# Kernel tuning notes

Measured on AMD Instinct MI355X. Metric: run time of the kernel, lower is better.

## Reference

```python
import jax, jax.numpy as jnp
import numpy as np

N, E, DIM, L, NPERM, B = 20000, 640000, 128, 4, 20000, 256
R = NPERM * L * L  # rows of perm matrices
EPS = 1e-5


def _mlp(x, w1, b1, g, beta, w2, b2):
    # Linear -> BatchNorm (training-mode batch stats) -> ReLU -> Linear
    h = x @ w1 + b1
    mu = h.mean(0)
    var = h.var(0)  # biased, matches torch BN normalization
    h = (h - mu) * jax.lax.rsqrt(var + EPS) * g + beta
    return jax.nn.relu(h) @ w2 + b2


def setup_inputs() -> dict:
    key = jax.random.key(0)
    ks = jax.random.split(key, 40)
    s = 0.05
    inp = {}
    inp["node_feat"] = jax.random.normal(ks[0], (N, DIM), jnp.float32)
    inp["edge_feat"] = jax.random.normal(ks[1], (E, DIM), jnp.float32)
    inp["src"] = jax.random.randint(ks[2], (E,), 0, N)
    inp["dst"] = jax.random.randint(ks[3], (E,), 0, N)
    inp["rev_flag"] = jax.random.randint(ks[4], (E,), 0, 2).astype(bool)
    # sparse node_to_perm / edge_to_perm: one nnz per row (row i implicit)
    inp["n2p_cols"] = jax.random.randint(ks[5], (R,), 0, N)
    inp["n2p_vals"] = jax.random.uniform(ks[6], (R,), jnp.float32)
    inp["e2p_cols"] = jax.random.randint(ks[7], (R,), 0, E)
    inp["e2p_vals"] = jax.random.uniform(ks[8], (R,), jnp.float32)
    # sparse pooling matrix: perm j -> graph pool_rows[j] with weight pool_vals[j]
    inp["pool_rows"] = jax.random.randint(ks[9], (NPERM,), 0, B)
    inp["pool_vals"] = jax.random.uniform(ks[10], (NPERM,), jnp.float32)
    for i, n in enumerate(["in_w", "out_w", "src_w", "dst_w", "nloop_w", "eloop_w"]):
        inp[n] = jax.random.normal(ks[11 + i], (DIM, DIM), jnp.float32) * s
    inp["lrp_w"] = jax.random.normal(ks[17], (DIM, DIM, L * L), jnp.float32) * s
    inp["nbias"] = jnp.zeros((DIM,), jnp.float32)
    inp["ebias"] = jnp.zeros((DIM,), jnp.float32)
    inp["lrp_bias"] = jnp.zeros((DIM,), jnp.float32)
    for p, k0 in (("n", 20), ("e", 26)):
        inp[p + "mlp_w1"] = jax.random.normal(ks[k0], (DIM, DIM), jnp.float32) * s
        inp[p + "mlp_b1"] = jnp.zeros((DIM,), jnp.float32)
        inp[p + "mlp_g"] = jnp.ones((DIM,), jnp.float32)
        inp[p + "mlp_beta"] = jnp.zeros((DIM,), jnp.float32)
        inp[p + "mlp_w2"] = jax.random.normal(ks[k0 + 1], (DIM, DIM), jnp.float32) * s
        inp[p + "mlp_b2"] = jnp.zeros((DIM,), jnp.float32)
    return inp


def reference(node_feat, edge_feat, src, dst, rev_flag, n2p_cols, n2p_vals,
              e2p_cols, e2p_vals, pool_rows, pool_vals,
              in_w, out_w, src_w, dst_w, nloop_w, eloop_w, lrp_w,
              nbias, ebias, lrp_bias,
              nmlp_w1, nmlp_b1, nmlp_g, nmlp_beta, nmlp_w2, nmlp_b2,
              emlp_w1, emlp_b1, emlp_g, emlp_beta, emlp_w2, emlp_b2):
    hs = node_feat[src]   # [E, d]
    hd = node_feat[dst]   # [E, d]
    r = rev_flag[:, None]
    # per-edge messages with reverse-edge masking
    edge_msg = jnp.where(r, hs @ dst_w - hd @ src_w, hd @ dst_w - hs @ src_w)
    node_msg = jnp.where(r, edge_feat @ out_w, -(edge_feat @ in_w))
    node_agg = jax.ops.segment_sum(node_msg, dst, num_segments=N)
    # node update
    nout = _mlp(node_feat @ nloop_w + node_agg + nbias,
                nmlp_w1, nmlp_b1, nmlp_g, nmlp_beta, nmlp_w2, nmlp_b2)
    # edge update: degree-scaled term uses out-degree of dst node
    out_deg = jax.ops.segment_sum(jnp.ones((E,), jnp.float32), src, num_segments=N)
    dlog = jnp.log2(1.0 + out_deg[dst])[:, None]
    add = 2.0 * (1.0 + dlog) * (edge_feat @ (src_w - dst_w))
    eout = _mlp(edge_feat @ eloop_w + add + edge_msg + ebias,
                emlp_w1, emlp_b1, emlp_g, emlp_beta, emlp_w2, emlp_b2)
    # sparse perm gathers + LRP einsum + sparse pooling scatter
    perm = n2p_vals[:, None] * nout[n2p_cols] + e2p_vals[:, None] * eout[e2p_cols]
    perm = perm.reshape(NPERM, L * L, DIM)
    lrp = jnp.einsum('dab,bca->dc', perm, lrp_w) + lrp_bias
    pooled = jax.ops.segment_sum(pool_vals[:, None] * lrp, pool_rows, num_segments=B)
    return pooled, eout
```

## Files before the change

kernel.cpp:

```cpp
#include <hip/hip_runtime.h>
#include <stdint.h>

constexpr int Nn     = 20000;
constexpr int Ee     = 640000;
constexpr int NPERMc = 20000;

using bf16x8 = __attribute__((ext_vector_type(8))) short;
using f32x4  = __attribute__((ext_vector_type(4))) float;
using s16x4  = __attribute__((ext_vector_type(4))) short;
using u16x8  = __attribute__((ext_vector_type(8))) unsigned short;

__device__ __forceinline__ short f2bf(float f) {
  union { float f; unsigned u; } v; v.f = f;
  unsigned r = v.u + 0x7FFFu + ((v.u >> 16) & 1u);
  return (short)(r >> 16);
}
__device__ __forceinline__ float bf2f(unsigned short s) {
  union { unsigned u; float f; } v; v.u = ((unsigned)s) << 16;
  return v.f;
}
__device__ __forceinline__ f32x4 MFMA(bf16x8 a, bf16x8 b, f32x4 c) {
  return __builtin_amdgcn_mfma_f32_16x16x32_bf16(a, b, c, 0, 0, 0);
}

__device__ __forceinline__ int fragIdx(int k, int n) {
  int t = n >> 4, kk = k >> 5;
  int l = ((k & 31) >> 3) * 16 + (n & 15);
  int j = k & 7;
  return ((t * 4 + kk) * 64 + l) * 8 + j;
}

__device__ __forceinline__ void stage16x128(const float* __restrict__ src, int row0, int M,
                                            int lane, short* lds) {
  #pragma unroll
  for (int it = 0; it < 8; ++it) {
    int u = it * 64 + lane;
    int r = u >> 5;
    int q = u & 31;
    int row = row0 + r;
    float4 v = make_float4(0.f, 0.f, 0.f, 0.f);
    if (row < M) v = ((const float4*)(src + (size_t)row * 128))[q];
    int k  = q * 4;
    int kk = k >> 5;
    int l2 = ((k & 31) >> 3) * 16 + r;
    int j  = k & 7;
    s16x4 s4 = { f2bf(v.x), f2bf(v.y), f2bf(v.z), f2bf(v.w) };
    *(s16x4*)(lds + (kk * 64 + l2) * 8 + j) = s4;
  }
}

__global__ __launch_bounds__(256) void kPrep(
    const float* __restrict__ in_w,  const float* __restrict__ out_w,
    const float* __restrict__ src_w, const float* __restrict__ dst_w,
    const float* __restrict__ nloop_w, const float* __restrict__ eloop_w,
    const float* __restrict__ lrp_w,
    const float* __restrict__ nbias, const float* __restrict__ ebias,
    const float* __restrict__ w1e, const float* __restrict__ b1e,
    const float* __restrict__ w1n, const float* __restrict__ b1n,
    const float* __restrict__ w2e, const float* __restrict__ w2n,
    short* __restrict__ WA, short* __restrict__ BQ, short* __restrict__ WN,
    short* __restrict__ W2E, short* __restrict__ W2N, short* __restrict__ WL,
    float* __restrict__ c0e, float* __restrict__ c0n) {
  __shared__ float Rl[16384];
  int tid = threadIdx.x;
  int blk = blockIdx.x;
  if (blk < 448) {
    int p = blk >> 6, sub = blk & 63;
    const float* La; const float* Lb = nullptr; const float* R; short* outp;
    float sOut = 1.f;
    switch (p) {
      case 0: La = eloop_w;             R = w1e; outp = WA;          break;
      case 1: La = src_w; Lb = dst_w;   R = w1e; outp = WA + 16384;  break;
      case 2: La = dst_w;               R = w1e; outp = BQ;          break;
      case 3: La = src_w;               R = w1e; outp = BQ + 16384;  break;
      case 4: La = nloop_w;             R = w1n; outp = WN;          break;
      case 5: La = out_w;               R = w1n; outp = WN + 16384;  break;
      default: La = in_w;               R = w1n; outp = WN + 32768; sOut = -1.f; break;
    }
    for (int i = tid; i < 16384; i += 256) Rl[i] = R[i];
    __syncthreads();
    int e = sub * 256 + tid;
    int k = e >> 7, n = e & 127;
    float acc = 0.f;
    bool hasLb = (Lb != nullptr);
    for (int j = 0; j < 128; ++j) {
      float l = La[k * 128 + j];
      if (hasLb) l -= Lb[k * 128 + j];
      acc += l * Rl[j * 128 + n];
    }
    outp[fragIdx(k, n)] = f2bf(acc * sOut);
  } else if (blk < 512) {
    int e = (blk - 448) * 256 + tid; int k = e >> 7, n = e & 127;
    W2E[fragIdx(k, n)] = f2bf(w2e[k * 128 + n]);
  } else if (blk < 576) {
    int e = (blk - 512) * 256 + tid; int k = e >> 7, n = e & 127;
    W2N[fragIdx(k, n)] = f2bf(w2n[k * 128 + n]);
  } else if (blk < 1600) {
    int q = blk - 576; int a = q >> 6;
    int e = (q & 63) * 256 + tid; int k = e >> 7, n = e & 127;
    WL[a * 16384 + fragIdx(k, n)] = f2bf(lrp_w[(k * 128 + n) * 16 + a]);
  } else {
    if (tid < 128) {
      float acc = 0.f;
      for (int k2 = 0; k2 < 128; ++k2) acc += ebias[k2] * w1e[k2 * 128 + tid];
      c0e[tid] = acc + b1e[tid];
    } else {
      int n = tid - 128; float acc = 0.f;
      for (int k2 = 0; k2 < 128; ++k2) acc += nbias[k2] * w1n[k2 * 128 + n];
      c0n[n] = acc + b1n[n];
    }
  }
}


__global__ __launch_bounds__(256) void kHist(
    const int* __restrict__ srcI, const int* __restrict__ dstI,
    int* __restrict__ cnt, float* __restrict__ deg) {
  int e = blockIdx.x * 256 + threadIdx.x;
  atomicAdd(&cnt[dstI[e]], 1);
  atomicAdd(&deg[srcI[e]], 1.0f);
}

__global__ __launch_bounds__(256) void kScan(const int* __restrict__ cnt,
                                             int* __restrict__ off,
                                             int* __restrict__ cur) {
  __shared__ int lc[Nn];
  __shared__ int ps[256];
  int tid = threadIdx.x;
  for (int i = tid; i < Nn; i += 256) lc[i] = cnt[i];
  __syncthreads();
  constexpr int CH = (Nn + 255) / 256;
  int base = tid * CH;
  int local = 0;
  for (int i = 0; i < CH; ++i) {
    int idx = base + i;
    if (idx < Nn) local += lc[idx];
  }
  ps[tid] = local;
  __syncthreads();
  for (int d = 1; d < 256; d <<= 1) {
    int t = (tid >= d) ? ps[tid - d] : 0;
    __syncthreads();
    if (tid >= d) ps[tid] += t;
    __syncthreads();
  }
  int run = ps[tid] - local;
  for (int i = 0; i < CH; ++i) {
    int idx = base + i;
    if (idx < Nn) { off[idx] = run; cur[idx] = run; run += lc[idx]; }
  }
}

__global__ __launch_bounds__(256) void kScatter(
    const int* __restrict__ dstI, const int* __restrict__ revI,
    int* __restrict__ cur, int* __restrict__ order) {
  int e = blockIdx.x * 256 + threadIdx.x;
  int pos = atomicAdd(&cur[dstI[e]], 1);
  order[pos] = revI[e] ? (e | (int)0x80000000) : e;
}

__global__ __launch_bounds__(256) void kAgg2(
    const float* __restrict__ ef, const int* __restrict__ off,
    const int* __restrict__ cnt, const int* __restrict__ order,
    float* __restrict__ aggR, float* __restrict__ aggN) {
  int w = threadIdx.x >> 6, lane = threadIdx.x & 63;
  int n = blockIdx.x * 4 + w;
  if (n >= Nn) return;
  int s0 = off[n], c = cnt[n];
  float2 aR = make_float2(0.f, 0.f), aN = make_float2(0.f, 0.f);
  int i = 0;
  for (; i + 1 < c; i += 2) {
    int oe0 = order[s0 + i];
    int oe1 = order[s0 + i + 1];
    int e0 = oe0 & 0x7fffffff;
    int e1 = oe1 & 0x7fffffff;
    float2 v0 = ((const float2*)(ef + (size_t)e0 * 128))[lane];
    float2 v1 = ((const float2*)(ef + (size_t)e1 * 128))[lane];
    if (oe0 < 0) { aR.x += v0.x; aR.y += v0.y; } else { aN.x += v0.x; aN.y += v0.y; }
    if (oe1 < 0) { aR.x += v1.x; aR.y += v1.y; } else { aN.x += v1.x; aN.y += v1.y; }
  }
  if (i < c) {
    int oe = order[s0 + i];
    int e = oe & 0x7fffffff;
    float2 v = ((const float2*)(ef + (size_t)e * 128))[lane];
    if (oe < 0) { aR.x += v.x; aR.y += v.y; } else { aN.x += v.x; aN.y += v.y; }
  }
  ((float2*)(aggR + (size_t)n * 128))[lane] = aR;
  ((float2*)(aggN + (size_t)n * 128))[lane] = aN;
}

__global__ __launch_bounds__(256, 2) void kQ(const float* __restrict__ nf,
                                             const short* __restrict__ BQ,
                                             float* __restrict__ Q, int M) {
  __shared__ __align__(16) short alds[4][2048];
  __shared__ __align__(16) short wbuf[8192];
  int tid = threadIdx.x, w = tid >> 6, lane = tid & 63;
  int row0 = blockIdx.x * 64 + w * 16;
  stage16x128(nf, row0, M, lane, alds[w]);
  f32x4 acc[16];
  #pragma unroll
  for (int t = 0; t < 16; ++t) acc[t] = (f32x4){0.f, 0.f, 0.f, 0.f};
  const int4* g4 = (const int4*)BQ;
  for (int kk = 0; kk < 4; ++kk) {
    __syncthreads();
    for (int c = tid; c < 1024; c += 256) {
      int t = c >> 6, l = c & 63;
      ((int4*)wbuf)[c] = g4[(t * 4 + kk) * 64 + l];
    }
    __syncthreads();
    bf16x8 a = *(const bf16x8*)(alds[w] + (kk * 64 + lane) * 8);
    #pragma unroll
    for (int t = 0; t < 16; ++t) {
      bf16x8 b = *(const bf16x8*)(wbuf + (t * 64 + lane) * 8);
      acc[t] = MFMA(a, b, acc[t]);
    }
  }
  int sub = lane >> 4;
  #pragma unroll
  for (int t = 0; t < 16; ++t) {
    int col = t * 16 + (lane & 15);
    #pragma unroll
    for (int i = 0; i < 4; ++i) {
      int row = row0 + sub * 4 + i;
      if (row < M) Q[(size_t)row * 256 + col] = acc[t][i];
    }
  }
}

__global__ __launch_bounds__(256, 2) void kN1(
    const float* __restrict__ nf, const float* __restrict__ aggR,
    const float* __restrict__ aggN, const short* __restrict__ WN,
    const float* __restrict__ c0n, short* __restrict__ hN,
    float* __restrict__ scratchN, int M) {
  __shared__ __align__(16) short alds[4][2048];
  __shared__ __align__(16) short wlds[16384];
  __shared__ float statsLDS[256];
  int tid = threadIdx.x, w = tid >> 6, lane = tid & 63;
  statsLDS[tid] = 0.f;
  int row0 = blockIdx.x * 64 + w * 16;
  f32x4 acc[8];
  #pragma unroll
  for (int t = 0; t < 8; ++t) acc[t] = (f32x4){0.f, 0.f, 0.f, 0.f};
  for (int s = 0; s < 3; ++s) {
    const float* src = (s == 0) ? nf : ((s == 1) ? aggR : aggN);
    __syncthreads();
    const int4* g4 = (const int4*)(WN + s * 16384);
    for (int c = tid; c < 2048; c += 256) ((int4*)wlds)[c] = g4[c];
    __syncthreads();
    stage16x128(src, row0, M, lane, alds[w]);
    for (int kk = 0; kk < 4; ++kk) {
      bf16x8 a = *(const bf16x8*)(alds[w] + (kk * 64 + lane) * 8);
      #pragma unroll
      for (int t = 0; t < 8; ++t) {
        bf16x8 b = *(const bf16x8*)(wlds + ((t * 4 + kk) * 64 + lane) * 8);
        acc[t] = MFMA(a, b, acc[t]);
      }
    }
  }
  int sub = lane >> 4;
  #pragma unroll
  for (int t = 0; t < 8; ++t) {
    int col = t * 16 + (lane & 15);
    float c0 = c0n[col];
    float ss = 0.f, sq = 0.f;
    #pragma unroll
    for (int i = 0; i < 4; ++i) {
      int row = row0 + sub * 4 + i;
      float h = acc[t][i] + c0;
      if (row < M) { hN[(size_t)row * 128 + col] = f2bf(h); ss += h; sq += h * h; }
    }
    ss += __shfl_xor(ss, 16, 64); sq += __shfl_xor(sq, 16, 64);
    ss += __shfl_xor(ss, 32, 64); sq += __shfl_xor(sq, 32, 64);
    if (lane < 16) { atomicAdd(&statsLDS[col], ss); atomicAdd(&statsLDS[128 + col], sq); }
  }
  __syncthreads();
  scratchN[(size_t)tid * gridDim.x + blockIdx.x] = statsLDS[tid];
}

__global__ __launch_bounds__(256, 2) void kD(
    const float* __restrict__ ef, const short* __restrict__ WA,
    const float* __restrict__ Q, const float* __restrict__ c0e,
    const int* __restrict__ srcI, const int* __restrict__ dstI,
    const int* __restrict__ revI, const float* __restrict__ deg,
    short* __restrict__ hE, float* __restrict__ scratchE) {
  __shared__ __align__(16) short alds[4][4096];
  __shared__ __align__(16) short wbuf[4096];
  __shared__ float statsLDS[256];
  int tid = threadIdx.x, w = tid >> 6, lane = tid & 63;
  statsLDS[tid] = 0.f;
  int row0 = blockIdx.x * 128 + w * 32;
  stage16x128(ef, row0,      Ee, lane, alds[w]);
  stage16x128(ef, row0 + 16, Ee, lane, alds[w] + 2048);
  f32x4 acc1[2][8], acc2[2][8];
  #pragma unroll
  for (int g = 0; g < 2; ++g)
    #pragma unroll
    for (int t = 0; t < 8; ++t) { acc1[g][t] = (f32x4){0,0,0,0}; acc2[g][t] = (f32x4){0,0,0,0}; }
  const int4* g4 = (const int4*)WA;
  for (int kk = 0; kk < 4; ++kk) {
    bf16x8 a0 = *(const bf16x8*)(alds[w] + (kk * 64 + lane) * 8);
    bf16x8 a1 = *(const bf16x8*)(alds[w] + 2048 + (kk * 64 + lane) * 8);
    #pragma unroll
    for (int m = 0; m < 2; ++m) {
      __syncthreads();
      for (int c = tid; c < 512; c += 256) {
        int t = c >> 6, l = c & 63;
        ((int4*)wbuf)[c] = g4[m * 2048 + (t * 4 + kk) * 64 + l];
      }
      __syncthreads();
      #pragma unroll
      for (int t = 0; t < 8; ++t) {
        bf16x8 b = *(const bf16x8*)(wbuf + (t * 64 + lane) * 8);
        if (m == 0) { acc1[0][t] = MFMA(a0, b, acc1[0][t]); acc1[1][t] = MFMA(a1, b, acc1[1][t]); }
        else        { acc2[0][t] = MFMA(a0, b, acc2[0][t]); acc2[1][t] = MFMA(a1, b, acc2[1][t]); }
      }
    }
  }
  int sub = lane >> 4;
  #pragma unroll
  for (int g = 0; g < 2; ++g) {
    int rbase = row0 + g * 16;
    int   eIdx[4]; float scl[4]; int qa[4], qb[4];
    #pragma unroll
    for (int i = 0; i < 4; ++i) {
      int e = rbase + sub * 4 + i;
      eIdx[i] = e;
      int s_ = srcI[e], d_ = dstI[e], r_ = revI[e];
      scl[i] = 2.0f * (1.0f + log2f(1.0f + deg[d_]));
      int na = r_ ? s_ : d_;
      int nb = r_ ? d_ : s_;
      qa[i] = na * 256;
      qb[i] = nb * 256 + 128;
    }
    #pragma unroll
    for (int t = 0; t < 8; ++t) {
      int col = t * 16 + (lane & 15);
      float c0 = c0e[col];
      float ss = 0.f, sq = 0.f;
      #pragma unroll
      for (int i = 0; i < 4; ++i) {
        float h = acc1[g][t][i] + scl[i] * acc2[g][t][i]
                + (Q[qa[i] + col] - Q[qb[i] + col]) + c0;
        hE[(size_t)eIdx[i] * 128 + col] = f2bf(h);
        ss += h; sq += h * h;
      }
      ss += __shfl_xor(ss, 16, 64); sq += __shfl_xor(sq, 16, 64);
      ss += __shfl_xor(ss, 32, 64); sq += __shfl_xor(sq, 32, 64);
      if (lane < 16) { atomicAdd(&statsLDS[col], ss); atomicAdd(&statsLDS[128 + col], sq); }
    }
  }
  __syncthreads();
  scratchE[(size_t)tid * gridDim.x + blockIdx.x] = statsLDS[tid];
}

__global__ __launch_bounds__(256) void kFin(const float* __restrict__ scratch, int NB,
                                            float M, const float* __restrict__ g,
                                            const float* __restrict__ beta,
                                            float* __restrict__ st) {
  __shared__ float red[256];
  __shared__ float red2[256];
  int c = blockIdx.x;
  int tid = threadIdx.x;
  float s = 0.f, q = 0.f;
  for (int i = tid; i < NB; i += 256) {
    s += scratch[(size_t)c * NB + i];
    q += scratch[(size_t)(128 + c) * NB + i];
  }
  red[tid] = s; red2[tid] = q;
  __syncthreads();
  for (int off = 128; off > 0; off >>= 1) {
    if (tid < off) { red[tid] += red[tid + off]; red2[tid] += red2[tid + off]; }
    __syncthreads();
  }
  if (tid == 0) {
    float mu  = red[0] / M;
    float var = red2[0] / M - mu * mu;
    float inv = rsqrtf(var + 1e-5f);
    float sc  = g[c] * inv;
    st[c] = sc;
    st[128 + c] = beta[c] - mu * sc;
  }
}

__global__ __launch_bounds__(256, 2) void kF(const short* __restrict__ h,
                                             const float* __restrict__ st,
                                             const short* __restrict__ w2f,
                                             const float* __restrict__ b2,
                                             float* __restrict__ outp, int M) {
  __shared__ __align__(16) short alds[4][2048];
  __shared__ __align__(16) short wlds[16384];
  int tid = threadIdx.x, w = tid >> 6, lane = tid & 63;
  for (int c = tid; c < 2048; c += 256) ((int4*)wlds)[c] = ((const int4*)w2f)[c];
  int row0 = blockIdx.x * 64 + w * 16;
  #pragma unroll
  for (int it = 0; it < 4; ++it) {
    int u = it * 64 + lane;
    int r = u >> 4;
    int c8 = (u & 15) * 8;
    int row = row0 + r;
    u16x8 hv = {0, 0, 0, 0, 0, 0, 0, 0};
    if (row < M) hv = *(const u16x8*)(h + (size_t)row * 128 + c8);
    bf16x8 ov;
    #pragma unroll
    for (int q = 0; q < 8; ++q) {
      float f = bf2f(hv[q]);
      float v = fmaxf(f * st[c8 + q] + st[128 + c8 + q], 0.f);
      ov[q] = f2bf(v);
    }
    int kk = c8 >> 5;
    int l2 = ((c8 & 31) >> 3) * 16 + r;
    *(bf16x8*)(alds[w] + (kk * 64 + l2) * 8) = ov;
  }
  __syncthreads();
  f32x4 acc[8];
  #pragma unroll
  for (int t = 0; t < 8; ++t) acc[t] = (f32x4){0.f, 0.f, 0.f, 0.f};
  for (int kk = 0; kk < 4; ++kk) {
    bf16x8 a = *(const bf16x8*)(alds[w] + (kk * 64 + lane) * 8);
    #pragma unroll
    for (int t = 0; t < 8; ++t) {
      bf16x8 b = *(const bf16x8*)(wlds + ((t * 4 + kk) * 64 + lane) * 8);
      acc[t] = MFMA(a, b, acc[t]);
    }
  }
  int sub = lane >> 4;
  #pragma unroll
  for (int t = 0; t < 8; ++t) {
    int col = t * 16 + (lane & 15);
    float bb = b2[col];
    #pragma unroll
    for (int i = 0; i < 4; ++i) {
      int row = row0 + sub * 4 + i;
      if (row < M) outp[(size_t)row * 128 + col] = acc[t][i] + bb;
    }
  }
}

__global__ __launch_bounds__(256, 2) void kLRP(
    const float* __restrict__ nout, const float* __restrict__ eoutp,
    const int* __restrict__ n2pc, const float* __restrict__ n2pv,
    const int* __restrict__ e2pc, const float* __restrict__ e2pv,
    const int* __restrict__ poolr, const float* __restrict__ poolv,
    const short* __restrict__ WL, const float* __restrict__ lrp_bias,
    float* __restrict__ pooled) {
  __shared__ __align__(16) short alds[4][2048];
  __shared__ __align__(16) short wlds[16384];
  int tid = threadIdx.x, w = tid >> 6, lane = tid & 63;
  int row0 = blockIdx.x * 64 + w * 16;
  f32x4 acc[8];
  #pragma unroll
  for (int t = 0; t < 8; ++t) acc[t] = (f32x4){0.f, 0.f, 0.f, 0.f};
  for (int a = 0; a < 16; ++a) {
    __syncthreads();
    const int4* g4 = (const int4*)(WL + a * 16384);
    for (int c = tid; c < 2048; c += 256) ((int4*)wlds)[c] = g4[c];
    __syncthreads();
    #pragma unroll
    for (int it = 0; it < 8; ++it) {
      int u = it * 64 + lane;
      int r = u >> 5;
      int q = u & 31;
      int d = row0 + r;
      float4 v = make_float4(0.f, 0.f, 0.f, 0.f);
      if (d < NPERMc) {
        int i = d * 16 + a;
        int nc = n2pc[i]; float nv = n2pv[i];
        int ec = e2pc[i]; float ev = e2pv[i];
        float4 nr = ((const float4*)(nout  + (size_t)nc * 128))[q];
        float4 er = ((const float4*)(eoutp + (size_t)ec * 128))[q];
        v.x = nv * nr.x + ev * er.x;
        v.y = nv * nr.y + ev * er.y;
        v.z = nv * nr.z + ev * er.z;
        v.w = nv * nr.w + ev * er.w;
      }
      int k  = q * 4;
      int kk = k >> 5;
      int l2 = ((k & 31) >> 3) * 16 + r;
      int j  = k & 7;
      s16x4 s4 = { f2bf(v.x), f2bf(v.y), f2bf(v.z), f2bf(v.w) };
      *(s16x4*)(alds[w] + (kk * 64 + l2) * 8 + j) = s4;
    }
    for (int kk = 0; kk < 4; ++kk) {
      bf16x8 aa = *(const bf16x8*)(alds[w] + (kk * 64 + lane) * 8);
      #pragma unroll
      for (int t = 0; t < 8; ++t) {
        bf16x8 b = *(const bf16x8*)(wlds + ((t * 4 + kk) * 64 + lane) * 8);
        acc[t] = MFMA(aa, b, acc[t]);
      }
    }
  }
  int sub = lane >> 4;
  #pragma unroll
  for (int t = 0; t < 8; ++t) {
    int col = t * 16 + (lane & 15);
    float lb = lrp_bias[col];
    #pragma unroll
    for (int i = 0; i < 4; ++i) {
      int d = row0 + sub * 4 + i;
      if (d < NPERMc) {
        float val = acc[t][i] + lb;
        atomicAdd(&pooled[poolr[d] * 128 + col], poolv[d] * val);
      }
    }
  }
}

extern "C" void kernel_launch(void* const* d_in, const int* in_sizes, int n_in,
                              void* d_out, int out_size, void* d_ws, size_t ws_size,
                              hipStream_t stream) {
  (void)in_sizes; (void)n_in; (void)out_size; (void)ws_size;
  const float* node_feat = (const float*)d_in[0];
  const float* edge_feat = (const float*)d_in[1];
  const int*   srcI      = (const int*)d_in[2];
  const int*   dstI      = (const int*)d_in[3];
  const int*   revI      = (const int*)d_in[4];
  const int*   n2pc      = (const int*)d_in[5];
  const float* n2pv      = (const float*)d_in[6];
  const int*   e2pc      = (const int*)d_in[7];
  const float* e2pv      = (const float*)d_in[8];
  const int*   poolr     = (const int*)d_in[9];
  const float* poolv     = (const float*)d_in[10];
  const float* in_w      = (const float*)d_in[11];
  const float* out_w     = (const float*)d_in[12];
  const float* src_w     = (const float*)d_in[13];
  const float* dst_w     = (const float*)d_in[14];
  const float* nloop_w   = (const float*)d_in[15];
  const float* eloop_w   = (const float*)d_in[16];
  const float* lrp_w     = (const float*)d_in[17];
  const float* nbias     = (const float*)d_in[18];
  const float* ebias     = (const float*)d_in[19];
  const float* lrp_bias  = (const float*)d_in[20];
  const float* nmlp_w1   = (const float*)d_in[21];
  const float* nmlp_b1   = (const float*)d_in[22];
  const float* nmlp_g    = (const float*)d_in[23];
  const float* nmlp_beta = (const float*)d_in[24];
  const float* nmlp_w2   = (const float*)d_in[25];
  const float* nmlp_b2   = (const float*)d_in[26];
  const float* emlp_w1   = (const float*)d_in[27];
  const float* emlp_b1   = (const float*)d_in[28];
  const float* emlp_g    = (const float*)d_in[29];
  const float* emlp_beta = (const float*)d_in[30];
  const float* emlp_w2   = (const float*)d_in[31];
  const float* emlp_b2   = (const float*)d_in[32];

  float* pooled = (float*)d_out;
  float* eoutp  = (float*)d_out + 32768;

  char* p = (char*)d_ws;
  auto alloc = [&](size_t b) { char* r = p; p += (b + 255) & ~(size_t)255; return r; };
  short* hE   = (short*)alloc((size_t)Ee * 128 * 2);
  float* Qm   = (float*)alloc((size_t)Nn * 256 * 4);
  float* aggR = (float*)alloc((size_t)Nn * 128 * 4);
  float* aggN = (float*)alloc((size_t)Nn * 128 * 4);
  short* hN   = (short*)alloc((size_t)Nn * 128 * 2);
  float* nout = (float*)alloc((size_t)Nn * 128 * 4);
  float* deg  = (float*)alloc((size_t)Nn * 4);
  float* scrE = (float*)alloc((size_t)256 * 5000 * 4);
  float* scrN = (float*)alloc((size_t)256 * 313 * 4);
  float* stE  = (float*)alloc(256 * 4);
  float* stN  = (float*)alloc(256 * 4);
  short* WA   = (short*)alloc(32768 * 2);
  short* BQ   = (short*)alloc(32768 * 2);
  short* WN   = (short*)alloc(49152 * 2);
  short* W2E  = (short*)alloc(16384 * 2);
  short* W2N  = (short*)alloc(16384 * 2);
  short* WL   = (short*)alloc((size_t)16 * 16384 * 2);
  float* c0e  = (float*)alloc(128 * 4);
  float* c0n  = (float*)alloc(128 * 4);
  int*   cnt  = (int*)alloc((size_t)Nn * 4);
  int*   offA = (int*)alloc((size_t)Nn * 4);
  int*   cur  = (int*)alloc((size_t)Nn * 4);
  int*   order= (int*)alloc((size_t)Ee * 4);

  hipMemsetAsync(deg,  0, (size_t)Nn * 4, stream);
  hipMemsetAsync(cnt,  0, (size_t)Nn * 4, stream);
  hipMemsetAsync(pooled, 0, (size_t)32768 * 4, stream);

  kPrep<<<1601, 256, 0, stream>>>(in_w, out_w, src_w, dst_w, nloop_w, eloop_w, lrp_w,
                                  nbias, ebias, emlp_w1, emlp_b1, nmlp_w1, nmlp_b1,
                                  emlp_w2, nmlp_w2, WA, BQ, WN, W2E, W2N, WL, c0e, c0n);
  kHist<<<Ee / 256, 256, 0, stream>>>(srcI, dstI, cnt, deg);
  kScan<<<1, 256, 0, stream>>>(cnt, offA, cur);
  kScatter<<<Ee / 256, 256, 0, stream>>>(dstI, revI, cur, order);
  kAgg2<<<Nn / 4, 256, 0, stream>>>(edge_feat, offA, cnt, order, aggR, aggN);
  kQ<<<313, 256, 0, stream>>>(node_feat, BQ, Qm, Nn);
  kN1<<<313, 256, 0, stream>>>(node_feat, aggR, aggN, WN, c0n, hN, scrN, Nn);
  kD<<<5000, 256, 0, stream>>>(edge_feat, WA, Qm, c0e, srcI, dstI, revI, deg, hE, scrE);
  kFin<<<128, 256, 0, stream>>>(scrE, 5000, (float)Ee, emlp_g, emlp_beta, stE);
  kFin<<<128, 256, 0, stream>>>(scrN, 313, (float)Nn, nmlp_g, nmlp_beta, stN);
  kF<<<10000, 256, 0, stream>>>(hE, stE, W2E, emlp_b2, eoutp, Ee);
  kF<<<313, 256, 0, stream>>>(hN, stN, W2N, nmlp_b2, nout, Nn);
  kLRP<<<313, 256, 0, stream>>>(nout, eoutp, n2pc, n2pv, e2pc, e2pv,
                                poolr, poolv, WL, lrp_bias, pooled);
}
```

Measured before the change: 1.455 ms.

## Permute Q layout for vector gathers and drop LDS weight staging in kD

kQ now writes Q in a per-lane permuted column order, so kD can fetch each edge's two gathered Q rows with float4 loads instead of scalar strided loads. kD is split into half-size blocks (64 edges), twice as many blocks, and higher occupancy via launch bounds. B fragments are read straight from global memory rather than staged through LDS with barriers. The index and degree gathers are hoisted ahead of the MFMA loop so their latency can overlap the matrix work. The cost is more L2 traffic for weights, since every wave rereads them, and a larger per-block stats scratch for kFin to reduce.

```diff
diff --git a/kernel.cpp b/kernel.cpp
--- a/kernel.cpp
+++ b/kernel.cpp
@@ -215,14 +215,21 @@
       acc[t] = MFMA(a, b, acc[t]);
     }
   }
-  int sub = lane >> 4;
-  #pragma unroll
-  for (int t = 0; t < 16; ++t) {
-    int col = t * 16 + (lane & 15);
-    #pragma unroll
-    for (int i = 0; i < 4; ++i) {
-      int row = row0 + sub * 4 + i;
-      if (row < M) Q[(size_t)row * 256 + col] = acc[t][i];
+  int sub = lane >> 4, m = lane & 15;
+  #pragma unroll
+  for (int i = 0; i < 4; ++i) {
+    int row = row0 + sub * 4 + i;
+    if (row < M) {
+      #pragma unroll
+      for (int h = 0; h < 2; ++h) {
+        float4 f0, f1;
+        f0.x = acc[h * 8 + 0][i]; f0.y = acc[h * 8 + 1][i];
+        f0.z = acc[h * 8 + 2][i]; f0.w = acc[h * 8 + 3][i];
+        f1.x = acc[h * 8 + 4][i]; f1.y = acc[h * 8 + 5][i];
+        f1.z = acc[h * 8 + 6][i]; f1.w = acc[h * 8 + 7][i];
+        float4* dst = (float4*)(Q + (size_t)row * 256 + h * 128 + m * 8);
+        dst[0] = f0; dst[1] = f1;
+      }
     }
   }
 }
@@ -277,76 +284,76 @@
   scratchN[(size_t)tid * gridDim.x + blockIdx.x] = statsLDS[tid];
 }
 
-__global__ __launch_bounds__(256, 2) void kD(
+__global__ __launch_bounds__(256, 3) void kD(
     const float* __restrict__ ef, const short* __restrict__ WA,
     const float* __restrict__ Q, const float* __restrict__ c0e,
     const int* __restrict__ srcI, const int* __restrict__ dstI,
     const int* __restrict__ revI, const float* __restrict__ deg,
     short* __restrict__ hE, float* __restrict__ scratchE) {
-  __shared__ __align__(16) short alds[4][4096];
-  __shared__ __align__(16) short wbuf[4096];
+  __shared__ __align__(16) short alds[4][2048];
   __shared__ float statsLDS[256];
   int tid = threadIdx.x, w = tid >> 6, lane = tid & 63;
+  int m = lane & 15, sub = lane >> 4;
   statsLDS[tid] = 0.f;
-  int row0 = blockIdx.x * 128 + w * 32;
-  stage16x128(ef, row0,      Ee, lane, alds[w]);
-  stage16x128(ef, row0 + 16, Ee, lane, alds[w] + 2048);
-  f32x4 acc1[2][8], acc2[2][8];
-  #pragma unroll
-  for (int g = 0; g < 2; ++g)
-    #pragma unroll
-    for (int t = 0; t < 8; ++t) { acc1[g][t] = (f32x4){0,0,0,0}; acc2[g][t] = (f32x4){0,0,0,0}; }
-  const int4* g4 = (const int4*)WA;
+  __syncthreads();
+  int row0 = blockIdx.x * 64 + w * 16;
+  float scl[4]; int qa[4], qb[4];
+  #pragma unroll
+  for (int i = 0; i < 4; ++i) {
+    int e = row0 + sub * 4 + i;
+    int s_ = srcI[e], d_ = dstI[e], r_ = revI[e];
+    scl[i] = 2.0f * (1.0f + log2f(1.0f + deg[d_]));
+    int na = r_ ? s_ : d_;
+    int nb = r_ ? d_ : s_;
+    qa[i] = na * 256 + m * 8;
+    qb[i] = nb * 256 + 128 + m * 8;
+  }
+  stage16x128(ef, row0, Ee, lane, alds[w]);
+  f32x4 acc1[8], acc2[8];
+  #pragma unroll
+  for (int t = 0; t < 8; ++t) { acc1[t] = (f32x4){0,0,0,0}; acc2[t] = (f32x4){0,0,0,0}; }
+  const bf16x8* WB = (const bf16x8*)WA;
+  #pragma unroll
   for (int kk = 0; kk < 4; ++kk) {
-    bf16x8 a0 = *(const bf16x8*)(alds[w] + (kk * 64 + lane) * 8);
-    bf16x8 a1 = *(const bf16x8*)(alds[w] + 2048 + (kk * 64 + lane) * 8);
-    #pragma unroll
-    for (int m = 0; m < 2; ++m) {
-      __syncthreads();
-      for (int c = tid; c < 512; c += 256) {
-        int t = c >> 6, l = c & 63;
-        ((int4*)wbuf)[c] = g4[m * 2048 + (t * 4 + kk) * 64 + l];
-      }
-      __syncthreads();
-      #pragma unroll
-      for (int t = 0; t < 8; ++t) {
-        bf16x8 b = *(const bf16x8*)(wbuf + (t * 64 + lane) * 8);
-        if (m == 0) { acc1[0][t] = MFMA(a0, b, acc1[0][t]); acc1[1][t] = MFMA(a1, b, acc1[1][t]); }
-        else        { acc2[0][t] = MFMA(a0, b, acc2[0][t]); acc2[1][t] = MFMA(a1, b, acc2[1][t]); }
-      }
-    }
-  }
-  int sub = lane >> 4;
-  #pragma unroll
-  for (int g = 0; g < 2; ++g) {
-    int rbase = row0 + g * 16;
-    int   eIdx[4]; float scl[4]; int qa[4], qb[4];
-    #pragma unroll
-    for (int i = 0; i < 4; ++i) {
-      int e = rbase + sub * 4 + i;
-      eIdx[i] = e;
-      int s_ = srcI[e], d_ = dstI[e], r_ = revI[e];
-      scl[i] = 2.0f * (1.0f + log2f(1.0f + deg[d_]));
-      int na = r_ ? s_ : d_;
-      int nb = r_ ? d_ : s_;
-      qa[i] = na * 256;
-      qb[i] = nb * 256 + 128;
-    }
+    bf16x8 a = *(const bf16x8*)(alds[w] + (kk * 64 + lane) * 8);
     #pragma unroll
     for (int t = 0; t < 8; ++t) {
-      int col = t * 16 + (lane & 15);
-      float c0 = c0e[col];
-      float ss = 0.f, sq = 0.f;
-      #pragma unroll
-      for (int i = 0; i < 4; ++i) {
-        float h = acc1[g][t][i] + scl[i] * acc2[g][t][i]
-                + (Q[qa[i] + col] - Q[qb[i] + col]) + c0;
-        hE[(size_t)eIdx[i] * 128 + col] = f2bf(h);
-        ss += h; sq += h * h;
-      }
-      ss += __shfl_xor(ss, 16, 64); sq += __shfl_xor(sq, 16, 64);
-      ss += __shfl_xor(ss, 32, 64); sq += __shfl_xor(sq, 32, 64);
-      if (lane < 16) { atomicAdd(&statsLDS[col], ss); atomicAdd(&statsLDS[128 + col], sq); }
+      bf16x8 b1 = WB[(t * 4 + kk) * 64 + lane];
+      bf16x8 b2 = WB[2048 + (t * 4 + kk) * 64 + lane];
+      acc1[t] = MFMA(a, b1, acc1[t]);
+      acc2[t] = MFMA(a, b2, acc2[t]);
+    }
+  }
+  float c0[8];
+  #pragma unroll
+  for (int t = 0; t < 8; ++t) c0[t] = c0e[t * 16 + m];
+  float ss[8], sq[8];
+  #pragma unroll
+  for (int t = 0; t < 8; ++t) { ss[t] = 0.f; sq[t] = 0.f; }
+  #pragma unroll
+  for (int i = 0; i < 4; ++i) {
+    int e = row0 + sub * 4 + i;
+    float4 A0 = ((const float4*)(Q + qa[i]))[0];
+    float4 A1 = ((const float4*)(Q + qa[i]))[1];
+    float4 B0 = ((const float4*)(Q + qb[i]))[0];
+    float4 B1 = ((const float4*)(Q + qb[i]))[1];
+    float qv[8] = {A0.x - B0.x, A0.y - B0.y, A0.z - B0.z, A0.w - B0.w,
+                   A1.x - B1.x, A1.y - B1.y, A1.z - B1.z, A1.w - B1.w};
+    #pragma unroll
+    for (int t = 0; t < 8; ++t) {
+      float h = acc1[t][i] + scl[i] * acc2[t][i] + qv[t] + c0[t];
+      hE[(size_t)e * 128 + t * 16 + m] = f2bf(h);
+      ss[t] += h; sq[t] += h * h;
+    }
+  }
+  #pragma unroll
+  for (int t = 0; t < 8; ++t) {
+    float a = ss[t], b = sq[t];
+    a += __shfl_xor(a, 16, 64); b += __shfl_xor(b, 16, 64);
+    a += __shfl_xor(a, 32, 64); b += __shfl_xor(b, 32, 64);
+    if (lane < 16) {
+      atomicAdd(&statsLDS[t * 16 + lane], a);
+      atomicAdd(&statsLDS[128 + t * 16 + lane], b);
     }
   }
   __syncthreads();
@@ -555,7 +562,7 @@
   short* hN   = (short*)alloc((size_t)Nn * 128 * 2);
   float* nout = (float*)alloc((size_t)Nn * 128 * 4);
   float* deg  = (float*)alloc((size_t)Nn * 4);
-  float* scrE = (float*)alloc((size_t)256 * 5000 * 4);
+  float* scrE = (float*)alloc((size_t)256 * 10000 * 4);
   float* scrN = (float*)alloc((size_t)256 * 313 * 4);
   float* stE  = (float*)alloc(256 * 4);
   float* stN  = (float*)alloc(256 * 4);
@@ -585,8 +592,8 @@
   kAgg2<<<Nn / 4, 256, 0, stream>>>(edge_feat, offA, cnt, order, aggR, aggN);
   kQ<<<313, 256, 0, stream>>>(node_feat, BQ, Qm, Nn);
   kN1<<<313, 256, 0, stream>>>(node_feat, aggR, aggN, WN, c0n, hN, scrN, Nn);
-  kD<<<5000, 256, 0, stream>>>(edge_feat, WA, Qm, c0e, srcI, dstI, revI, deg, hE, scrE);
-  kFin<<<128, 256, 0, stream>>>(scrE, 5000, (float)Ee, emlp_g, emlp_beta, stE);
+  kD<<<10000, 256, 0, stream>>>(edge_feat, WA, Qm, c0e, srcI, dstI, revI, deg, hE, scrE);
+  kFin<<<128, 256, 0, stream>>>(scrE, 10000, (float)Ee, emlp_g, emlp_beta, stE);
   kFin<<<128, 256, 0, stream>>>(scrN, 313, (float)Nn, nmlp_g, nmlp_beta, stN);
   kF<<<10000, 256, 0, stream>>>(hE, stE, W2E, emlp_b2, eoutp, Ee);
   kF<<<313, 256, 0, stream>>>(hN, stN, W2N, nmlp_b2, nout, Nn);
```

Measured after the change: 1.497 ms. 1.03x slower.
